# Kernel optimization log

Hardware: AMD Instinct MI355X
Metric: run time of the kernel (lower is better)

Reference implementation:

```python
import jax, jax.numpy as jnp
import numpy as np
import math

N, B, D, K = 2000, 2000, 32, 3  # nodes, bills, dim, order+1


def setup_inputs() -> dict:
    key = jax.random.key(0)
    ks = jax.random.split(key, 6)
    return {
        "events": jax.random.randint(ks[0], (N, B), 0, 2) > 0,          # [N,B] bool votes
        "events_time": jax.random.uniform(ks[1], (B,), dtype=jnp.float32),  # [B] bill times
        "beta": jax.random.uniform(ks[2], (B,), dtype=jnp.float32),     # bill bias
        "gamma": jax.random.uniform(ks[3], (N,), dtype=jnp.float32),    # politician bias
        "z_b": jax.random.uniform(ks[4], (B, D), dtype=jnp.float32),    # bill embeddings
        "z_p": jax.random.uniform(ks[5], (K, N, D), dtype=jnp.float32), # stacked order-o politician coeffs
    }


def reference(events, events_time, beta, gamma, z_b, z_p):
    k = z_p.shape[0]
    inv_fact = jnp.asarray([1.0 / math.factorial(o) for o in range(k)], dtype=z_p.dtype)
    # powers[o, b] = t_b**o  (o=0 handled explicitly so grads are safe at t=0)
    powers = jnp.stack(
        [jnp.ones_like(events_time) if o == 0 else events_time ** o for o in range(k)]
    )  # [K,B]
    coeff = powers * inv_fact[:, None]                     # [K,B]  t^o/o!
    pos = jnp.einsum('kb,knd->bnd', coeff, z_p)            # [B,N,D] politician positions at each bill time
    diff = pos - z_b[:, None, :]                           # [B,N,D]
    dist = jnp.sqrt(jnp.sum(diff * diff, axis=-1))         # [B,N] Euclidean distance
    logits = gamma[None, :] + beta[:, None] - dist         # [B,N]
    # log p if voted, log(1-p) otherwise; log(1-sigmoid(x)) == log_sigmoid(-x)
    ll = jnp.where(events.T, jax.nn.log_sigmoid(logits), jax.nn.log_sigmoid(-logits))
    return -jnp.sum(ll)
```

## Files before the change

kernel.cpp:

```cpp
#include <hip/hip_runtime.h>
#include <hip/hip_fp16.h>
#include <math.h>

#define NN    2000
#define NB    2000
#define DD    32
#define NOCT  16
#define TILE  64
#define GDIM  32
#define NPART (GDIM * GDIM)

typedef _Float16 half8   __attribute__((ext_vector_type(8)));
typedef _Float16 half4   __attribute__((ext_vector_type(4)));
typedef float    float4v __attribute__((ext_vector_type(4)));

__device__ __forceinline__ float dot4(const float4 a, const float4 b) {
    return fmaf(a.x, b.x, fmaf(a.y, b.y, fmaf(a.z, b.z, a.w * b.w)));
}
__device__ __forceinline__ half4 cvt4(const float x, const float y,
                                      const float z, const float w) {
    half4 h; h[0] = (_Float16)x; h[1] = (_Float16)y;
    h[2] = (_Float16)z; h[3] = (_Float16)w; return h;
}

__global__ __launch_bounds__(256, 4) void pol2vec_main(
    const int*   __restrict__ events,
    const float* __restrict__ tarr,
    const float* __restrict__ beta,
    const float* __restrict__ gamma,
    const float* __restrict__ zb,
    const float* __restrict__ zp,
    float*       __restrict__ partials)
{
    __shared__ _Float16 sW[NOCT * TILE * 8];
    __shared__ _Float16 sZ[NOCT * TILE * 8];
    __shared__ float    s_red[4];

    const int tid  = threadIdx.x;
    const int lane = tid & 63;
    const int w    = tid >> 6;
    const int b0   = blockIdx.x * TILE;
    const int n0   = blockIdx.y * TILE;
    const int wr   = (w >> 1) * 32;
    const int wc   = (w & 1) * 32;
    const int l15  = lane & 15;
    const int l4   = lane >> 4;

    unsigned evb = 0u, vb = 0u;
#pragma unroll
    for (int nr = 0; nr < 2; ++nr)
#pragma unroll
    for (int bc = 0; bc < 2; ++bc)
#pragma unroll
    for (int r = 0; r < 4; ++r) {
        const int ng = n0 + wr + 16 * nr + l4 * 4 + r;
        const int bg = b0 + wc + 16 * bc + l15;
        const bool v = (ng < NN) && (bg < NB);
        const size_t idx = v ? ((size_t)ng * NB + bg) : 0;
        const unsigned bit = 1u << (nr * 8 + bc * 4 + r);
        if (v) vb |= bit;
        if (v && events[idx]) evb |= bit;
    }

    if (tid < 3 * TILE) {
        const half8 zz = {};
        *(half8*)(sW + ((size_t)(13 * TILE + tid)) * 8) = zz;
        *(half8*)(sZ + ((size_t)(13 * TILE + tid)) * 8) = zz;
    }

    const int row = tid >> 3;
    const int q   = tid & 7;
    const int hs  = (q & 1) * 4;

#pragma unroll
    for (int p = 0; p < 2; ++p) {
        const int nl = 32 * p + row;
        const int n  = n0 + nl;
        float4 a4 = {0.f,0.f,0.f,0.f}, b4 = {0.f,0.f,0.f,0.f}, c4 = {0.f,0.f,0.f,0.f};
        if (n < NN) {
            a4 = ((const float4*)(zp + (size_t)n * DD))[q];
            b4 = ((const float4*)(zp + ((size_t)NN + n) * DD))[q];
            c4 = ((const float4*)(zp + ((size_t)2 * NN + n) * DD))[q];
        }
        *(half4*)(sW + ((size_t)((0 + (q >> 1)) * TILE + nl)) * 8 + hs) =
            cvt4(a4.x, a4.y, a4.z, a4.w);
        *(half4*)(sW + ((size_t)((4 + (q >> 1)) * TILE + nl)) * 8 + hs) =
            cvt4(b4.x, b4.y, b4.z, b4.w);
        *(half4*)(sW + ((size_t)((8 + (q >> 1)) * TILE + nl)) * 8 + hs) =
            cvt4(c4.x, c4.y, c4.z, c4.w);

        float paa = dot4(a4, a4), pab = dot4(a4, b4), pac = dot4(a4, c4);
        float pbb = dot4(b4, b4), pbc = dot4(b4, c4), pcc = dot4(c4, c4);
#pragma unroll
        for (int off = 1; off < 8; off <<= 1) {
            paa += __shfl_xor(paa, off); pab += __shfl_xor(pab, off);
            pac += __shfl_xor(pac, off); pbb += __shfl_xor(pbb, off);
            pbc += __shfl_xor(pbc, off); pcc += __shfl_xor(pcc, off);
        }
        if (q == 0) {
            half8 hv = {};
            hv[0] = (_Float16)paa;
            hv[1] = (_Float16)(2.f * pab);
            hv[2] = (_Float16)(pbb + pac);
            hv[3] = (_Float16)pbc;
            hv[4] = (_Float16)(0.25f * pcc);
            hv[5] = (_Float16)1.f;
            *(half8*)(sW + ((size_t)(12 * TILE + nl)) * 8) = hv;
        }
    }

#pragma unroll
    for (int p = 0; p < 2; ++p) {
        const int bl = 32 * p + row;
        const int b  = b0 + bl;
        float4 z4 = {0.f,0.f,0.f,0.f};
        float t = 0.f;
        if (b < NB) {
            z4 = ((const float4*)(zb + (size_t)b * DD))[q];
            t  = tarr[b];
        }
        const float th = 0.5f * t * t;
        *(half4*)(sZ + ((size_t)((0 + (q >> 1)) * TILE + bl)) * 8 + hs) =
            cvt4(z4.x, z4.y, z4.z, z4.w);
        *(half4*)(sZ + ((size_t)((4 + (q >> 1)) * TILE + bl)) * 8 + hs) =
            cvt4(t * z4.x, t * z4.y, t * z4.z, t * z4.w);
        *(half4*)(sZ + ((size_t)((8 + (q >> 1)) * TILE + bl)) * 8 + hs) =
            cvt4(th * z4.x, th * z4.y, th * z4.z, th * z4.w);

        float pz2 = dot4(z4, z4);
#pragma unroll
        for (int off = 1; off < 8; off <<= 1) pz2 += __shfl_xor(pz2, off);
        if (q == 0) {
            const float t2 = t * t;
            half8 hv = {};
            hv[0] = (_Float16)(-0.5f);
            hv[1] = (_Float16)(-0.5f * t);
            hv[2] = (_Float16)(-0.5f * t2);
            hv[3] = (_Float16)(-0.5f * t2 * t);
            hv[4] = (_Float16)(-0.5f * t2 * t2);
            hv[5] = (_Float16)(-0.5f * pz2);
            *(half8*)(sZ + ((size_t)(12 * TILE + bl)) * 8) = hv;
        }
    }
    __syncthreads();

    half8 af[2][4], bf[2][4];
#pragma unroll
    for (int ks = 0; ks < 4; ++ks) {
        const int oct = 4 * ks + l4;
#pragma unroll
        for (int h = 0; h < 2; ++h) {
            af[h][ks] = *(const half8*)(sW + ((size_t)oct * TILE + wr + 16 * h + l15) * 8);
            bf[h][ks] = *(const half8*)(sZ + ((size_t)oct * TILE + wc + 16 * h + l15) * 8);
        }
    }

    float4v acc[2][2] = {};
#pragma unroll
    for (int nr = 0; nr < 2; ++nr)
#pragma unroll
    for (int bc = 0; bc < 2; ++bc)
#pragma unroll
    for (int ks = 0; ks < 4; ++ks)
        acc[nr][bc] = __builtin_amdgcn_mfma_f32_16x16x32_f16(
            af[nr][ks], bf[bc][ks], acc[nr][bc], 0, 0, 0);

    float accs = 0.f;
#pragma unroll
    for (int bc = 0; bc < 2; ++bc) {
        const int bg = b0 + wc + 16 * bc + l15;
        const float be = beta[bg < NB ? bg : 0];
#pragma unroll
        for (int nr = 0; nr < 2; ++nr) {
#pragma unroll
            for (int r = 0; r < 4; ++r) {
                const int ng = n0 + wr + 16 * nr + l4 * 4 + r;
                const float g = gamma[ng < NN ? ng : 0];
                const float d2 = fmaxf(-2.f * acc[nr][bc][r], 0.f);
                const float L  = g + be - sqrtf(d2);
                const unsigned bit = 1u << (nr * 8 + bc * 4 + r);
                const float sgn = (evb & bit) ? 1.f : -1.f;
                const float s   = sgn * L;
                const float term = fmaxf(-s, 0.f) + __logf(1.f + __expf(-fabsf(s)));
                accs += (vb & bit) ? term : 0.f;
            }
        }
    }

#pragma unroll
    for (int o = 32; o > 0; o >>= 1) accs += __shfl_down(accs, o, 64);
    if (lane == 0) s_red[w] = accs;
    __syncthreads();
    if (tid == 0)
        partials[blockIdx.y * GDIM + blockIdx.x] =
            (s_red[0] + s_red[1]) + (s_red[2] + s_red[3]);
}

__global__ __launch_bounds__(256) void pol2vec_reduce(
    const float4* __restrict__ p4, float* __restrict__ out)
{
    __shared__ float s_red[4];
    const int tid = threadIdx.x;
    const float4 v = p4[tid];
    float s = (v.x + v.y) + (v.z + v.w);
#pragma unroll
    for (int o = 32; o > 0; o >>= 1) s += __shfl_down(s, o, 64);
    if ((tid & 63) == 0) s_red[tid >> 6] = s;
    __syncthreads();
    if (tid == 0) out[0] = (s_red[0] + s_red[1]) + (s_red[2] + s_red[3]);
}

extern "C" void kernel_launch(void* const* d_in, const int* in_sizes, int n_in,
                              void* d_out, int out_size, void* d_ws, size_t ws_size,
                              hipStream_t stream) {
    const int*   events = (const int*)d_in[0];
    const float* tarr   = (const float*)d_in[1];
    const float* beta   = (const float*)d_in[2];
    const float* gamma  = (const float*)d_in[3];
    const float* zb     = (const float*)d_in[4];
    const float* zp     = (const float*)d_in[5];
    float* out = (float*)d_out;

    float* parts = (float*)d_ws;

    dim3 grid(GDIM, GDIM);
    pol2vec_main<<<grid, 256, 0, stream>>>(events, tarr, beta, gamma, zb, zp,
                                           parts);
    pol2vec_reduce<<<1, 256, 0, stream>>>((const float4*)parts, out);
}
```

Before: 20.46 us.

## Process two bill tiles per block to reuse politician LDS fragments

Each block now covers 128 bills instead of 64, staging two bill tiles in shared memory and looping over them while keeping the politician A-fragments in registers. The grid's x dimension is halved to 16, so there are half as many blocks and half as many partial sums, and the reduce kernel now reads float2 instead of float4. The aim is to amortize the politician staging (loads, fp16 conversion, norm reductions) and per-block launch overhead across more work. In exchange, launch bounds drop to 2 waves and only 512 blocks remain, which lowers occupancy and parallelism on a 256-CU device.

```diff
diff --git a/kernel.cpp b/kernel.cpp
--- a/kernel.cpp
+++ b/kernel.cpp
@@ -7,8 +7,9 @@
 #define DD    32
 #define NOCT  16
 #define TILE  64
-#define GDIM  32
-#define NPART (GDIM * GDIM)
+#define GDX   16
+#define GDY   32
+#define NPART (GDX * GDY)
 
 typedef _Float16 half8   __attribute__((ext_vector_type(8)));
 typedef _Float16 half4   __attribute__((ext_vector_type(4)));
@@ -23,7 +24,7 @@
     h[2] = (_Float16)z; h[3] = (_Float16)w; return h;
 }
 
-__global__ __launch_bounds__(256, 4) void pol2vec_main(
+__global__ __launch_bounds__(256, 2) void pol2vec_main(
     const int*   __restrict__ events,
     const float* __restrict__ tarr,
     const float* __restrict__ beta,
@@ -33,20 +34,22 @@
     float*       __restrict__ partials)
 {
     __shared__ _Float16 sW[NOCT * TILE * 8];
-    __shared__ _Float16 sZ[NOCT * TILE * 8];
+    __shared__ _Float16 sZ[2][NOCT * TILE * 8];
     __shared__ float    s_red[4];
 
     const int tid  = threadIdx.x;
     const int lane = tid & 63;
     const int w    = tid >> 6;
-    const int b0   = blockIdx.x * TILE;
+    const int b0   = blockIdx.x * (2 * TILE);
     const int n0   = blockIdx.y * TILE;
     const int wr   = (w >> 1) * 32;
     const int wc   = (w & 1) * 32;
     const int l15  = lane & 15;
     const int l4   = lane >> 4;
 
-    unsigned evb = 0u, vb = 0u;
+    unsigned evb[2] = {0u, 0u}, vb[2] = {0u, 0u};
+#pragma unroll
+    for (int tau = 0; tau < 2; ++tau)
 #pragma unroll
     for (int nr = 0; nr < 2; ++nr)
 #pragma unroll
@@ -54,18 +57,19 @@
 #pragma unroll
     for (int r = 0; r < 4; ++r) {
         const int ng = n0 + wr + 16 * nr + l4 * 4 + r;
-        const int bg = b0 + wc + 16 * bc + l15;
+        const int bg = b0 + tau * TILE + wc + 16 * bc + l15;
         const bool v = (ng < NN) && (bg < NB);
         const size_t idx = v ? ((size_t)ng * NB + bg) : 0;
         const unsigned bit = 1u << (nr * 8 + bc * 4 + r);
-        if (v) vb |= bit;
-        if (v && events[idx]) evb |= bit;
+        if (v) vb[tau] |= bit;
+        if (v && events[idx]) evb[tau] |= bit;
     }
 
     if (tid < 3 * TILE) {
         const half8 zz = {};
-        *(half8*)(sW + ((size_t)(13 * TILE + tid)) * 8) = zz;
-        *(half8*)(sZ + ((size_t)(13 * TILE + tid)) * 8) = zz;
+        *(half8*)(sW    + ((size_t)(13 * TILE + tid)) * 8) = zz;
+        *(half8*)(sZ[0] + ((size_t)(13 * TILE + tid)) * 8) = zz;
+        *(half8*)(sZ[1] + ((size_t)(13 * TILE + tid)) * 8) = zz;
     }
 
     const int row = tid >> 3;
@@ -110,9 +114,11 @@
     }
 
 #pragma unroll
-    for (int p = 0; p < 2; ++p) {
-        const int bl = 32 * p + row;
-        const int b  = b0 + bl;
+    for (int p = 0; p < 4; ++p) {
+        const int bl  = 32 * p + row;
+        const int tau = bl >> 6;
+        const int r64 = bl & 63;
+        const int b   = b0 + bl;
         float4 z4 = {0.f,0.f,0.f,0.f};
         float t = 0.f;
         if (b < NB) {
@@ -120,11 +126,12 @@
             t  = tarr[b];
         }
         const float th = 0.5f * t * t;
-        *(half4*)(sZ + ((size_t)((0 + (q >> 1)) * TILE + bl)) * 8 + hs) =
+        _Float16* base = sZ[tau];
+        *(half4*)(base + ((size_t)((0 + (q >> 1)) * TILE + r64)) * 8 + hs) =
             cvt4(z4.x, z4.y, z4.z, z4.w);
-        *(half4*)(sZ + ((size_t)((4 + (q >> 1)) * TILE + bl)) * 8 + hs) =
+        *(half4*)(base + ((size_t)((4 + (q >> 1)) * TILE + r64)) * 8 + hs) =
             cvt4(t * z4.x, t * z4.y, t * z4.z, t * z4.w);
-        *(half4*)(sZ + ((size_t)((8 + (q >> 1)) * TILE + bl)) * 8 + hs) =
+        *(half4*)(base + ((size_t)((8 + (q >> 1)) * TILE + r64)) * 8 + hs) =
             cvt4(th * z4.x, th * z4.y, th * z4.z, th * z4.w);
 
         float pz2 = dot4(z4, z4);
@@ -139,50 +146,60 @@
             hv[3] = (_Float16)(-0.5f * t2 * t);
             hv[4] = (_Float16)(-0.5f * t2 * t2);
             hv[5] = (_Float16)(-0.5f * pz2);
-            *(half8*)(sZ + ((size_t)(12 * TILE + bl)) * 8) = hv;
+            *(half8*)(base + ((size_t)(12 * TILE + r64)) * 8) = hv;
         }
     }
     __syncthreads();
 
-    half8 af[2][4], bf[2][4];
+    half8 af[2][4];
 #pragma unroll
     for (int ks = 0; ks < 4; ++ks) {
         const int oct = 4 * ks + l4;
 #pragma unroll
-        for (int h = 0; h < 2; ++h) {
+        for (int h = 0; h < 2; ++h)
             af[h][ks] = *(const half8*)(sW + ((size_t)oct * TILE + wr + 16 * h + l15) * 8);
-            bf[h][ks] = *(const half8*)(sZ + ((size_t)oct * TILE + wc + 16 * h + l15) * 8);
-        }
-    }
-
-    float4v acc[2][2] = {};
-#pragma unroll
-    for (int nr = 0; nr < 2; ++nr)
-#pragma unroll
-    for (int bc = 0; bc < 2; ++bc)
-#pragma unroll
-    for (int ks = 0; ks < 4; ++ks)
-        acc[nr][bc] = __builtin_amdgcn_mfma_f32_16x16x32_f16(
-            af[nr][ks], bf[bc][ks], acc[nr][bc], 0, 0, 0);
+    }
 
     float accs = 0.f;
 #pragma unroll
-    for (int bc = 0; bc < 2; ++bc) {
-        const int bg = b0 + wc + 16 * bc + l15;
-        const float be = beta[bg < NB ? bg : 0];
-#pragma unroll
-        for (int nr = 0; nr < 2; ++nr) {
-#pragma unroll
-            for (int r = 0; r < 4; ++r) {
-                const int ng = n0 + wr + 16 * nr + l4 * 4 + r;
-                const float g = gamma[ng < NN ? ng : 0];
-                const float d2 = fmaxf(-2.f * acc[nr][bc][r], 0.f);
-                const float L  = g + be - sqrtf(d2);
-                const unsigned bit = 1u << (nr * 8 + bc * 4 + r);
-                const float sgn = (evb & bit) ? 1.f : -1.f;
-                const float s   = sgn * L;
-                const float term = fmaxf(-s, 0.f) + __logf(1.f + __expf(-fabsf(s)));
-                accs += (vb & bit) ? term : 0.f;
+    for (int tau = 0; tau < 2; ++tau) {
+        half8 bf[2][4];
+#pragma unroll
+        for (int ks = 0; ks < 4; ++ks) {
+            const int oct = 4 * ks + l4;
+#pragma unroll
+            for (int h = 0; h < 2; ++h)
+                bf[h][ks] = *(const half8*)(sZ[tau] + ((size_t)oct * TILE + wc + 16 * h + l15) * 8);
+        }
+
+        float4v acc[2][2] = {};
+#pragma unroll
+        for (int nr = 0; nr < 2; ++nr)
+#pragma unroll
+        for (int bc = 0; bc < 2; ++bc)
+#pragma unroll
+        for (int ks = 0; ks < 4; ++ks)
+            acc[nr][bc] = __builtin_amdgcn_mfma_f32_16x16x32_f16(
+                af[nr][ks], bf[bc][ks], acc[nr][bc], 0, 0, 0);
+
+#pragma unroll
+        for (int bc = 0; bc < 2; ++bc) {
+            const int bg = b0 + tau * TILE + wc + 16 * bc + l15;
+            const float be = beta[bg < NB ? bg : 0];
+#pragma unroll
+            for (int nr = 0; nr < 2; ++nr) {
+#pragma unroll
+                for (int r = 0; r < 4; ++r) {
+                    const int ng = n0 + wr + 16 * nr + l4 * 4 + r;
+                    const float g = gamma[ng < NN ? ng : 0];
+                    const float d2 = fmaxf(-2.f * acc[nr][bc][r], 0.f);
+                    const float L  = g + be - sqrtf(d2);
+                    const unsigned bit = 1u << (nr * 8 + bc * 4 + r);
+                    const float sgn = (evb[tau] & bit) ? 1.f : -1.f;
+                    const float s   = sgn * L;
+                    const float term = fmaxf(-s, 0.f) + __logf(1.f + __expf(-fabsf(s)));
+                    accs += (vb[tau] & bit) ? term : 0.f;
+                }
             }
         }
     }
@@ -192,17 +209,17 @@
     if (lane == 0) s_red[w] = accs;
     __syncthreads();
     if (tid == 0)
-        partials[blockIdx.y * GDIM + blockIdx.x] =
+        partials[blockIdx.y * GDX + blockIdx.x] =
             (s_red[0] + s_red[1]) + (s_red[2] + s_red[3]);
 }
 
 __global__ __launch_bounds__(256) void pol2vec_reduce(
-    const float4* __restrict__ p4, float* __restrict__ out)
+    const float2* __restrict__ p2, float* __restrict__ out)
 {
     __shared__ float s_red[4];
     const int tid = threadIdx.x;
-    const float4 v = p4[tid];
-    float s = (v.x + v.y) + (v.z + v.w);
+    const float2 v = p2[tid];
+    float s = v.x + v.y;
 #pragma unroll
     for (int o = 32; o > 0; o >>= 1) s += __shfl_down(s, o, 64);
     if ((tid & 63) == 0) s_red[tid >> 6] = s;
@@ -223,8 +240,8 @@
 
     float* parts = (float*)d_ws;
 
-    dim3 grid(GDIM, GDIM);
+    dim3 grid(GDX, GDY);
     pol2vec_main<<<grid, 256, 0, stream>>>(events, tarr, beta, gamma, zb, zp,
                                            parts);
-    pol2vec_reduce<<<1, 256, 0, stream>>>((const float4*)parts, out);
-}
+    pol2vec_reduce<<<1, 256, 0, stream>>>((const float2*)parts, out);
+}
```

Measured after the change: 22.20 us. 8.5% more time.
